# Kernel tuning notes

Hardware: AMD Instinct MI355X
Metric: run time of the kernel (lower is better)

The kernel has to match this reference:

```python
import jax, jax.numpy as jnp
import numpy as np

B, L, CIN, COUT, NCH = 64, 8192, 128, 128, 64


def setup_inputs() -> dict:
    key = jax.random.key(0)
    k1, k2, k3, k4 = jax.random.split(key, 4)
    x = jax.random.normal(k1, (B, L, CIN), dtype=jnp.float32)
    channels = jax.random.randint(k2, (L,), 0, NCH, dtype=jnp.int64)
    # kaiming_uniform-ish scale for weight, uniform bias in [-1/sqrt(fan_in), 1/sqrt(fan_in)]
    wbound = jnp.sqrt(1.0 / CIN)
    weight = jax.random.uniform(k3, (NCH, COUT, CIN), dtype=jnp.float32, minval=-wbound, maxval=wbound)
    bias = jax.random.uniform(k4, (NCH, COUT), dtype=jnp.float32, minval=-wbound, maxval=wbound)
    return {"x": x, "channels": channels, "weight": weight, "bias": bias}


def reference(x, channels, weight, bias):
    # Gather per-site weights: (L, Cout, Cin), then batched matmul over L.
    Wg = weight[channels]            # (L, Cout, Cin)
    bg = bias[channels]              # (L, Cout)
    y = jnp.einsum('blc,loc->blo', x, Wg)  # (B, L, Cout)
    y = y + bg                        # broadcast over B
    y = jnp.tanh(y)                   # activation=True
    y = y + x                         # residual mode 1 (Cout == Cin)
    return (y, channels)
```

## Files before the change

### kernel.cpp

```cpp
#include <hip/hip_runtime.h>
#include <hip/hip_bf16.h>


#define BB   64
#define LL   8192
#define CIN  128
#define COUT 128

#define PA 136
#define PW 136

typedef __bf16 bf16x4 __attribute__((ext_vector_type(4)));
typedef __bf16 bf16x8 __attribute__((ext_vector_type(8)));
typedef float  f32x4  __attribute__((ext_vector_type(4)));

__device__ __forceinline__ int load_channel(const int* __restrict__ ch32, int l) {
    bool is64 = true;
    #pragma unroll
    for (int i = 1; i < 32; i += 2) is64 = is64 && (ch32[i] == 0);
    return is64 ? ch32[2 * l] : ch32[l];
}

__global__ __launch_bounds__(256, 3) void gather_gemm_kernel(
    const float* __restrict__ x,
    const int* __restrict__ channels,
    const float* __restrict__ weight,
    const float* __restrict__ bias,
    float* __restrict__ out)
{
    __shared__ __align__(16) __hip_bfloat16 sA[BB * PA];
    __shared__ __align__(16) __hip_bfloat16 sW[COUT * PW];

    const int l = blockIdx.x;
    const int t = threadIdx.x;
    const int ch = load_channel(channels, l);

    const float* xl = x + (size_t)l * CIN;
    #pragma unroll
    for (int i = 0; i < 8; ++i) {
        int c   = t + 256 * i;
        int row = c >> 5;
        int cc  = c & 31;
        float4 v = *(const float4*)(xl + (size_t)row * ((size_t)LL * CIN) + cc * 4);
        bf16x4 b4 = { (__bf16)v.x, (__bf16)v.y, (__bf16)v.z, (__bf16)v.w };
        *(bf16x4*)(&sA[row * PA + cc * 4]) = b4;
    }
    const float* wc = weight + (size_t)ch * (COUT * CIN);
    #pragma unroll
    for (int i = 0; i < 16; ++i) {
        int c   = t + 256 * i;
        int row = c >> 5;
        int cc  = c & 31;
        float4 v = *(const float4*)(wc + row * CIN + cc * 4);
        bf16x4 b4 = { (__bf16)v.x, (__bf16)v.y, (__bf16)v.z, (__bf16)v.w };
        *(bf16x4*)(&sW[row * PW + cc * 4]) = b4;
    }
    __syncthreads();

    const int wave = t >> 6;
    const int lane = t & 63;
    const int n0   = lane & 15;
    const int quad = lane >> 4;

    f32x4 acc[4][2];
    #pragma unroll
    for (int mi = 0; mi < 4; ++mi)
        #pragma unroll
        for (int nj = 0; nj < 2; ++nj)
            acc[mi][nj] = (f32x4){0.f, 0.f, 0.f, 0.f};

    #pragma unroll
    for (int ks = 0; ks < 4; ++ks) {
        const int k = ks * 32 + quad * 8;
        bf16x8 afr[4], bfr[2];
        #pragma unroll
        for (int mi = 0; mi < 4; ++mi) {
            int m = mi * 16 + n0;
            afr[mi] = *(const bf16x8*)(&sA[m * PA + k]);
        }
        #pragma unroll
        for (int nj = 0; nj < 2; ++nj) {
            int n = wave * 32 + nj * 16 + n0;
            bfr[nj] = *(const bf16x8*)(&sW[n * PW + k]);
        }
        #pragma unroll
        for (int mi = 0; mi < 4; ++mi)
            #pragma unroll
            for (int nj = 0; nj < 2; ++nj)
                acc[mi][nj] = __builtin_amdgcn_mfma_f32_16x16x32_bf16(
                    afr[mi], bfr[nj], acc[mi][nj], 0, 0, 0);
    }

    #pragma unroll
    for (int nj = 0; nj < 2; ++nj) {
        const int o  = wave * 32 + nj * 16 + n0;
        const float bv = bias[ch * COUT + o];
        #pragma unroll
        for (int mi = 0; mi < 4; ++mi) {
            #pragma unroll
            for (int r = 0; r < 4; ++r) {
                const int b = mi * 16 + quad * 4 + r;
                float v = acc[mi][nj][r] + bv;
                float e  = __expf(2.0f * v);
                float th = 1.0f - 2.0f * __builtin_amdgcn_rcpf(e + 1.0f);
                float res = (float)sA[b * PA + o];
                out[((size_t)b * LL + l) * COUT + o] = th + res;
            }
        }
    }
}

__global__ void chan_out_kernel(const int* __restrict__ channels,
                                float* __restrict__ out)
{
    int i = blockIdx.x * blockDim.x + threadIdx.x;
    int v = load_channel(channels, i);
    if (i < LL)
        out[(size_t)BB * LL * COUT + i] = (float)v;
}

extern "C" void kernel_launch(void* const* d_in, const int* in_sizes, int n_in,
                              void* d_out, int out_size, void* d_ws, size_t ws_size,
                              hipStream_t stream) {
    const float* x        = (const float*)d_in[0];
    const int*   channels = (const int*)d_in[1];
    const float* weight   = (const float*)d_in[2];
    const float* bias     = (const float*)d_in[3];
    float*       out      = (float*)d_out;

    gather_gemm_kernel<<<dim3(LL), dim3(256), 0, stream>>>(x, channels, weight, bias, out);
    chan_out_kernel<<<dim3(LL / 256), dim3(256), 0, stream>>>(channels, out);
}
```

Before: 498.1 us.

## Pre-convert weights to bf16, load weight fragments into registers, vectorize output stores

Adds a pre-pass that converts the full weight tensor to bf16 in the workspace, so each block loads its channel's weight MFMA fragments straight from global memory into registers. This removes the shared-memory weight tile. The GEMM operands are swapped so each lane's accumulator holds four consecutive output channels, which lets the epilogue use vector bias loads, vector residual reads and 16-byte float4 output stores. LDS use drops and the occupancy hint rises from 3 to 5, at the cost of an extra conversion launch and more VGPRs for the held weight fragments.

Result: no change. 491.1 us (-1.4%).

```diff
diff --git a/kernel.cpp b/kernel.cpp
--- a/kernel.cpp
+++ b/kernel.cpp
@@ -6,9 +6,9 @@
 #define LL   8192
 #define CIN  128
 #define COUT 128
+#define NCH  64
 
 #define PA 136
-#define PW 136
 
 typedef __bf16 bf16x4 __attribute__((ext_vector_type(4)));
 typedef __bf16 bf16x8 __attribute__((ext_vector_type(8)));
@@ -21,15 +21,27 @@
     return is64 ? ch32[2 * l] : ch32[l];
 }
 
-__global__ __launch_bounds__(256, 3) void gather_gemm_kernel(
+__global__ void convert_w_kernel(const float* __restrict__ w,
+                                 __hip_bfloat16* __restrict__ wb)
+{
+    int i = (blockIdx.x * 256 + threadIdx.x) * 8;
+    float4 a = *(const float4*)(w + i);
+    float4 b = *(const float4*)(w + i + 4);
+    bf16x8 r = { (__bf16)a.x, (__bf16)a.y, (__bf16)a.z, (__bf16)a.w,
+                 (__bf16)b.x, (__bf16)b.y, (__bf16)b.z, (__bf16)b.w };
+    *(bf16x8*)(wb + i) = r;
+}
+
+template<bool PRE>
+__global__ __launch_bounds__(256, 5) void gather_gemm_kernel(
     const float* __restrict__ x,
     const int* __restrict__ channels,
     const float* __restrict__ weight,
+    const __hip_bfloat16* __restrict__ wbf,
     const float* __restrict__ bias,
     float* __restrict__ out)
 {
     __shared__ __align__(16) __hip_bfloat16 sA[BB * PA];
-    __shared__ __align__(16) __hip_bfloat16 sW[COUT * PW];
 
     const int l = blockIdx.x;
     const int t = threadIdx.x;
@@ -45,67 +57,80 @@
         bf16x4 b4 = { (__bf16)v.x, (__bf16)v.y, (__bf16)v.z, (__bf16)v.w };
         *(bf16x4*)(&sA[row * PA + cc * 4]) = b4;
     }
-    const float* wc = weight + (size_t)ch * (COUT * CIN);
-    #pragma unroll
-    for (int i = 0; i < 16; ++i) {
-        int c   = t + 256 * i;
-        int row = c >> 5;
-        int cc  = c & 31;
-        float4 v = *(const float4*)(wc + row * CIN + cc * 4);
-        bf16x4 b4 = { (__bf16)v.x, (__bf16)v.y, (__bf16)v.z, (__bf16)v.w };
-        *(bf16x4*)(&sW[row * PW + cc * 4]) = b4;
-    }
-    __syncthreads();
 
     const int wave = t >> 6;
     const int lane = t & 63;
     const int n0   = lane & 15;
     const int quad = lane >> 4;
 
-    f32x4 acc[4][2];
+    bf16x8 wfr[2][4];
+    if constexpr (PRE) {
+        const __hip_bfloat16* wbc = wbf + (size_t)ch * (COUT * CIN);
+        #pragma unroll
+        for (int oi = 0; oi < 2; ++oi) {
+            int n = wave * 32 + oi * 16 + n0;
+            #pragma unroll
+            for (int ks = 0; ks < 4; ++ks)
+                wfr[oi][ks] = *(const bf16x8*)(wbc + n * CIN + ks * 32 + quad * 8);
+        }
+    }
+    __syncthreads();
+
+    if constexpr (!PRE) {
+        const float* wc = weight + (size_t)ch * (COUT * CIN);
+        #pragma unroll
+        for (int oi = 0; oi < 2; ++oi) {
+            int n = wave * 32 + oi * 16 + n0;
+            #pragma unroll
+            for (int ks = 0; ks < 4; ++ks) {
+                const float* p = wc + n * CIN + ks * 32 + quad * 8;
+                float4 a = *(const float4*)(p);
+                float4 b = *(const float4*)(p + 4);
+                wfr[oi][ks] = (bf16x8){ (__bf16)a.x, (__bf16)a.y, (__bf16)a.z, (__bf16)a.w,
+                                        (__bf16)b.x, (__bf16)b.y, (__bf16)b.z, (__bf16)b.w };
+            }
+        }
+    }
+
+    f32x4 acc[2][4];
     #pragma unroll
-    for (int mi = 0; mi < 4; ++mi)
+    for (int oi = 0; oi < 2; ++oi)
         #pragma unroll
-        for (int nj = 0; nj < 2; ++nj)
-            acc[mi][nj] = (f32x4){0.f, 0.f, 0.f, 0.f};
+        for (int bj = 0; bj < 4; ++bj)
+            acc[oi][bj] = (f32x4){0.f, 0.f, 0.f, 0.f};
 
     #pragma unroll
     for (int ks = 0; ks < 4; ++ks) {
         const int k = ks * 32 + quad * 8;
-        bf16x8 afr[4], bfr[2];
+        bf16x8 afr[4];
         #pragma unroll
-        for (int mi = 0; mi < 4; ++mi) {
-            int m = mi * 16 + n0;
-            afr[mi] = *(const bf16x8*)(&sA[m * PA + k]);
-        }
+        for (int bj = 0; bj < 4; ++bj)
+            afr[bj] = *(const bf16x8*)(&sA[(bj * 16 + n0) * PA + k]);
         #pragma unroll
-        for (int nj = 0; nj < 2; ++nj) {
-            int n = wave * 32 + nj * 16 + n0;
-            bfr[nj] = *(const bf16x8*)(&sW[n * PW + k]);
-        }
-        #pragma unroll
-        for (int mi = 0; mi < 4; ++mi)
+        for (int oi = 0; oi < 2; ++oi)
             #pragma unroll
-            for (int nj = 0; nj < 2; ++nj)
-                acc[mi][nj] = __builtin_amdgcn_mfma_f32_16x16x32_bf16(
-                    afr[mi], bfr[nj], acc[mi][nj], 0, 0, 0);
+            for (int bj = 0; bj < 4; ++bj)
+                acc[oi][bj] = __builtin_amdgcn_mfma_f32_16x16x32_bf16(
+                    wfr[oi][ks], afr[bj], acc[oi][bj], 0, 0, 0);
     }
 
     #pragma unroll
-    for (int nj = 0; nj < 2; ++nj) {
-        const int o  = wave * 32 + nj * 16 + n0;
-        const float bv = bias[ch * COUT + o];
+    for (int oi = 0; oi < 2; ++oi) {
+        const int o0 = wave * 32 + oi * 16 + quad * 4;
+        const f32x4 bv = *(const f32x4*)(bias + ch * COUT + o0);
         #pragma unroll
-        for (int mi = 0; mi < 4; ++mi) {
+        for (int bj = 0; bj < 4; ++bj) {
+            const int b = bj * 16 + n0;
+            const bf16x4 rb = *(const bf16x4*)(&sA[b * PA + o0]);
+            f32x4 v;
             #pragma unroll
             for (int r = 0; r < 4; ++r) {
-                const int b = mi * 16 + quad * 4 + r;
-                float v = acc[mi][nj][r] + bv;
-                float e  = __expf(2.0f * v);
+                float vv = acc[oi][bj][r] + bv[r];
+                float e  = __expf(2.0f * vv);
                 float th = 1.0f - 2.0f * __builtin_amdgcn_rcpf(e + 1.0f);
-                float res = (float)sA[b * PA + o];
-                out[((size_t)b * LL + l) * COUT + o] = th + res;
+                v[r] = th + (float)rb[r];
             }
+            *(f32x4*)(&out[((size_t)b * LL + l) * COUT + o0]) = v;
         }
     }
 }
@@ -128,6 +153,15 @@
     const float* bias     = (const float*)d_in[3];
     float*       out      = (float*)d_out;
 
-    gather_gemm_kernel<<<dim3(LL), dim3(256), 0, stream>>>(x, channels, weight, bias, out);
+    const size_t wbytes = (size_t)NCH * COUT * CIN * sizeof(__hip_bfloat16);
+    if (ws_size >= wbytes) {
+        __hip_bfloat16* wbf = (__hip_bfloat16*)d_ws;
+        convert_w_kernel<<<dim3(512), dim3(256), 0, stream>>>(weight, wbf);
+        gather_gemm_kernel<true><<<dim3(LL), dim3(256), 0, stream>>>(
+            x, channels, weight, wbf, bias, out);
+    } else {
+        gather_gemm_kernel<false><<<dim3(LL), dim3(256), 0, stream>>>(
+            x, channels, weight, nullptr, bias, out);
+    }
     chan_out_kernel<<<dim3(LL / 256), dim3(256), 0, stream>>>(channels, out);
 }
```
